# Performance work log

Hardware: AMD Instinct MI355X
Metric: run time of the kernel (lower is better)

Reference implementation:

```python
import jax, jax.numpy as jnp
import numpy as np

SMOOTH_COEF = 0.025
FLOOR = 1e-06
B, T, C = 64, 4096, 128


def setup_inputs() -> dict:
    key = jax.random.key(0)
    k1, = jax.random.split(key, 1)
    inputs = jax.random.uniform(k1, (B, T, C), dtype=jnp.float32)  # nonneg spectrogram-like
    alpha = jnp.full((C,), 0.98, dtype=jnp.float32)
    delta = jnp.full((C,), 2.0, dtype=jnp.float32)
    root = jnp.full((C,), 2.0, dtype=jnp.float32)
    return {"inputs": inputs, "alpha": alpha, "delta": delta, "root": root}


def _ema(x, s):
    # m_t = s*x_t + (1-s)*m_{t-1}, with h_{-1} = x_0 => m_0 = x_0.
    # Linear recurrence via associative scan: pairs (a_t, b_t), m_t = a_t*m_{t-1} + b_t.
    Bn, Tn, Cn = x.shape
    a = jnp.full((Tn,), 1.0 - s, dtype=x.dtype).at[0].set(0.0)
    a = jnp.broadcast_to(a[None, :, None], x.shape)
    b = (s * x).at[:, 0, :].set(x[:, 0, :])

    def comb(c1, c2):
        a1, b1 = c1
        a2, b2 = c2
        return (a1 * a2, a2 * b1 + b2)

    _, m = jax.lax.associative_scan(comb, (a, b), axis=1)
    return m


def reference(inputs, alpha, delta, root):
    alpha_c = jnp.minimum(alpha, 1.0)          # [C]
    root_c = jnp.maximum(root, 1.0)            # [C]
    m = _ema(inputs, SMOOTH_COEF)              # [B,T,C] EMA smoother
    one_over_root = 1.0 / root_c
    term1 = jnp.power(FLOOR + m, alpha_c)
    term2 = jnp.power(inputs / term1 + delta, one_over_root)
    term3 = jnp.power(delta, one_over_root)
    return term2 - term3
```

## Files before the change

kernel.cpp:

```cpp
#include <hip/hip_runtime.h>


constexpr int Bn = 64, Tn = 4096, Cn = 128;
constexpr int NC = 128;
constexpr int Lc = Tn / NC;
constexpr int KWIN = 32;
constexpr float SC  = 0.025f;
constexpr float OMS = 1.0f - SC;
constexpr float FLOORV = 1e-6f;

__host__ __device__ constexpr float chunk_decay() {
    float a = 1.0f;
    for (int i = 0; i < Lc; ++i) a *= OMS;
    return a;
}
constexpr float ACH = chunk_decay();


__global__ __launch_bounds__(256) void k_partial(const float* __restrict__ x,
                                                 float* __restrict__ endv) {
    int gid   = blockIdx.x * 256 + threadIdx.x;
    int cg    = gid & 31;
    int chunk = (gid >> 5) & (NC - 1);
    int b     = gid >> 12;

    const float4* xp = (const float4*)x + (size_t)(b * Tn + chunk * Lc) * (Cn / 4) + cg;

    float4 v = xp[0];
    float4 m;
    if (chunk == 0) {
        m = v;
    } else {
        m.x = SC * v.x; m.y = SC * v.y; m.z = SC * v.z; m.w = SC * v.w;
    }
#pragma unroll 8
    for (int t = 1; t < Lc; ++t) {
        v = xp[(size_t)t * (Cn / 4)];
        m.x = fmaf(OMS, m.x, SC * v.x);
        m.y = fmaf(OMS, m.y, SC * v.y);
        m.z = fmaf(OMS, m.z, SC * v.z);
        m.w = fmaf(OMS, m.w, SC * v.w);
    }
    ((float4*)endv)[(size_t)(b * NC + chunk) * (Cn / 4) + cg] = m;
}

__device__ __forceinline__ float pcen_elem(float x, float m, float al, float dl,
                                           float oor, float t3) {
    float lg   = log2f(FLOORV + m);
    float inv1 = exp2f(-al * lg);
    float base = fmaf(x, inv1, dl);
    return exp2f(oor * log2f(base)) - t3;
}

__global__ __launch_bounds__(256) void k_final(const float* __restrict__ x,
                                               const float* __restrict__ alpha,
                                               const float* __restrict__ delta,
                                               const float* __restrict__ root,
                                               const float* __restrict__ endv,
                                               float* __restrict__ out) {
    int gid   = blockIdx.x * 256 + threadIdx.x;
    int cg    = gid & 31;
    int chunk = (gid >> 5) & (NC - 1);
    int b     = gid >> 12;

    const float4* ep = (const float4*)endv + (size_t)b * NC * (Cn / 4) + cg;
    float4 acc = {0.f, 0.f, 0.f, 0.f};
    int jstart = chunk - KWIN; if (jstart < 0) jstart = 0;
    for (int j = jstart; j < chunk; ++j) {
        float4 e = ep[(size_t)j * (Cn / 4)];
        acc.x = fmaf(ACH, acc.x, e.x);
        acc.y = fmaf(ACH, acc.y, e.y);
        acc.z = fmaf(ACH, acc.z, e.z);
        acc.w = fmaf(ACH, acc.w, e.w);
    }

    int c0 = cg * 4;
    float4 al = *(const float4*)(alpha + c0);
    float4 dl = *(const float4*)(delta + c0);
    float4 rt = *(const float4*)(root + c0);
    al.x = fminf(al.x, 1.f); al.y = fminf(al.y, 1.f); al.z = fminf(al.z, 1.f); al.w = fminf(al.w, 1.f);
    rt.x = fmaxf(rt.x, 1.f); rt.y = fmaxf(rt.y, 1.f); rt.z = fmaxf(rt.z, 1.f); rt.w = fmaxf(rt.w, 1.f);
    float4 oor = {1.f / rt.x, 1.f / rt.y, 1.f / rt.z, 1.f / rt.w};
    float4 t3  = {exp2f(oor.x * log2f(dl.x)), exp2f(oor.y * log2f(dl.y)),
                  exp2f(oor.z * log2f(dl.z)), exp2f(oor.w * log2f(dl.w))};

    size_t xoff = (size_t)(b * Tn + chunk * Lc) * (Cn / 4) + cg;
    const float4* xp = (const float4*)x + xoff;
    float4*       op = (float4*)out + xoff;

    float4 v = xp[0];
    float4 m;
    if (chunk == 0) {
        m = v;
    } else {
        m.x = fmaf(OMS, acc.x, SC * v.x);
        m.y = fmaf(OMS, acc.y, SC * v.y);
        m.z = fmaf(OMS, acc.z, SC * v.z);
        m.w = fmaf(OMS, acc.w, SC * v.w);
    }
    float4 o;
    o.x = pcen_elem(v.x, m.x, al.x, dl.x, oor.x, t3.x);
    o.y = pcen_elem(v.y, m.y, al.y, dl.y, oor.y, t3.y);
    o.z = pcen_elem(v.z, m.z, al.z, dl.z, oor.z, t3.z);
    o.w = pcen_elem(v.w, m.w, al.w, dl.w, oor.w, t3.w);
    op[0] = o;

#pragma unroll 8
    for (int t = 1; t < Lc; ++t) {
        v = xp[(size_t)t * (Cn / 4)];
        m.x = fmaf(OMS, m.x, SC * v.x);
        m.y = fmaf(OMS, m.y, SC * v.y);
        m.z = fmaf(OMS, m.z, SC * v.z);
        m.w = fmaf(OMS, m.w, SC * v.w);
        o.x = pcen_elem(v.x, m.x, al.x, dl.x, oor.x, t3.x);
        o.y = pcen_elem(v.y, m.y, al.y, dl.y, oor.y, t3.y);
        o.z = pcen_elem(v.z, m.z, al.z, dl.z, oor.z, t3.z);
        o.w = pcen_elem(v.w, m.w, al.w, dl.w, oor.w, t3.w);
        op[(size_t)t * (Cn / 4)] = o;
    }
}

extern "C" void kernel_launch(void* const* d_in, const int* in_sizes, int n_in,
                              void* d_out, int out_size, void* d_ws, size_t ws_size,
                              hipStream_t stream) {
    const float* x     = (const float*)d_in[0];
    const float* alpha = (const float*)d_in[1];
    const float* delta = (const float*)d_in[2];
    const float* root  = (const float*)d_in[3];
    float* out = (float*)d_out;
    float* ws  = (float*)d_ws;

    const int total = Bn * NC * (Cn / 4);
    k_partial<<<total / 256, 256, 0, stream>>>(x, ws);
    k_final<<<total / 256, 256, 0, stream>>>(x, alpha, delta, root, ws, out);
}
```

Baseline: 274.8 us.

## Halve chunk length, use raw amdgcn transcendentals and nontemporal output stores

Doubles the number of chunks so each thread scans 16 timesteps instead of 32, increasing thread count and memory parallelism. It also replaces libm log2/exp2 with the raw hardware builtins, writes output with nontemporal stores, and fully unrolls the loops. The truncated carry window stays at 32 chunks, so it now spans fewer timesteps, and the window-sum reads of chunk end values grow.

```diff
diff --git a/kernel.cpp b/kernel.cpp
--- a/kernel.cpp
+++ b/kernel.cpp
@@ -2,12 +2,14 @@
 
 
 constexpr int Bn = 64, Tn = 4096, Cn = 128;
-constexpr int NC = 128;
+constexpr int NC = 256;
 constexpr int Lc = Tn / NC;
 constexpr int KWIN = 32;
 constexpr float SC  = 0.025f;
 constexpr float OMS = 1.0f - SC;
 constexpr float FLOORV = 1e-6f;
+
+typedef float v4f __attribute__((ext_vector_type(4)));
 
 __host__ __device__ constexpr float chunk_decay() {
     float a = 1.0f;
@@ -22,7 +24,7 @@
     int gid   = blockIdx.x * 256 + threadIdx.x;
     int cg    = gid & 31;
     int chunk = (gid >> 5) & (NC - 1);
-    int b     = gid >> 12;
+    int b     = gid >> 13;
 
     const float4* xp = (const float4*)x + (size_t)(b * Tn + chunk * Lc) * (Cn / 4) + cg;
 
@@ -33,7 +35,7 @@
     } else {
         m.x = SC * v.x; m.y = SC * v.y; m.z = SC * v.z; m.w = SC * v.w;
     }
-#pragma unroll 8
+#pragma unroll
     for (int t = 1; t < Lc; ++t) {
         v = xp[(size_t)t * (Cn / 4)];
         m.x = fmaf(OMS, m.x, SC * v.x);
@@ -46,10 +48,10 @@
 
 __device__ __forceinline__ float pcen_elem(float x, float m, float al, float dl,
                                            float oor, float t3) {
-    float lg   = log2f(FLOORV + m);
-    float inv1 = exp2f(-al * lg);
+    float lg   = __builtin_amdgcn_logf(FLOORV + m);
+    float inv1 = __builtin_amdgcn_exp2f(-al * lg);
     float base = fmaf(x, inv1, dl);
-    return exp2f(oor * log2f(base)) - t3;
+    return __builtin_amdgcn_exp2f(oor * __builtin_amdgcn_logf(base)) - t3;
 }
 
 __global__ __launch_bounds__(256) void k_final(const float* __restrict__ x,
@@ -61,17 +63,29 @@
     int gid   = blockIdx.x * 256 + threadIdx.x;
     int cg    = gid & 31;
     int chunk = (gid >> 5) & (NC - 1);
-    int b     = gid >> 12;
+    int b     = gid >> 13;
 
     const float4* ep = (const float4*)endv + (size_t)b * NC * (Cn / 4) + cg;
     float4 acc = {0.f, 0.f, 0.f, 0.f};
-    int jstart = chunk - KWIN; if (jstart < 0) jstart = 0;
-    for (int j = jstart; j < chunk; ++j) {
-        float4 e = ep[(size_t)j * (Cn / 4)];
-        acc.x = fmaf(ACH, acc.x, e.x);
-        acc.y = fmaf(ACH, acc.y, e.y);
-        acc.z = fmaf(ACH, acc.z, e.z);
-        acc.w = fmaf(ACH, acc.w, e.w);
+    if (chunk >= KWIN) {
+        const float4* eb = ep + (size_t)(chunk - KWIN) * (Cn / 4);
+#pragma unroll
+        for (int j = 0; j < KWIN; ++j) {
+            float4 e = eb[(size_t)j * (Cn / 4)];
+            acc.x = fmaf(ACH, acc.x, e.x);
+            acc.y = fmaf(ACH, acc.y, e.y);
+            acc.z = fmaf(ACH, acc.z, e.z);
+            acc.w = fmaf(ACH, acc.w, e.w);
+        }
+    } else {
+#pragma unroll 8
+        for (int j = 0; j < chunk; ++j) {
+            float4 e = ep[(size_t)j * (Cn / 4)];
+            acc.x = fmaf(ACH, acc.x, e.x);
+            acc.y = fmaf(ACH, acc.y, e.y);
+            acc.z = fmaf(ACH, acc.z, e.z);
+            acc.w = fmaf(ACH, acc.w, e.w);
+        }
     }
 
     int c0 = cg * 4;
@@ -86,7 +100,7 @@
 
     size_t xoff = (size_t)(b * Tn + chunk * Lc) * (Cn / 4) + cg;
     const float4* xp = (const float4*)x + xoff;
-    float4*       op = (float4*)out + xoff;
+    v4f*          op = (v4f*)out + xoff;
 
     float4 v = xp[0];
     float4 m;
@@ -98,14 +112,14 @@
         m.z = fmaf(OMS, acc.z, SC * v.z);
         m.w = fmaf(OMS, acc.w, SC * v.w);
     }
-    float4 o;
+    v4f o;
     o.x = pcen_elem(v.x, m.x, al.x, dl.x, oor.x, t3.x);
     o.y = pcen_elem(v.y, m.y, al.y, dl.y, oor.y, t3.y);
     o.z = pcen_elem(v.z, m.z, al.z, dl.z, oor.z, t3.z);
     o.w = pcen_elem(v.w, m.w, al.w, dl.w, oor.w, t3.w);
-    op[0] = o;
+    __builtin_nontemporal_store(o, op);
 
-#pragma unroll 8
+#pragma unroll
     for (int t = 1; t < Lc; ++t) {
         v = xp[(size_t)t * (Cn / 4)];
         m.x = fmaf(OMS, m.x, SC * v.x);
@@ -116,7 +130,7 @@
         o.y = pcen_elem(v.y, m.y, al.y, dl.y, oor.y, t3.y);
         o.z = pcen_elem(v.z, m.z, al.z, dl.z, oor.z, t3.z);
         o.w = pcen_elem(v.w, m.w, al.w, dl.w, oor.w, t3.w);
-        op[(size_t)t * (Cn / 4)] = o;
+        __builtin_nontemporal_store(o, op + (size_t)t * (Cn / 4));
     }
 }
 
```

After: 260.7 us. -5.1%, faster.
